# Kernel optimization log

Measured on AMD Instinct MI355X. Metric: run time of the kernel, lower is better.

## Reference

```python
import jax, jax.numpy as jnp
import numpy as np


def _sliding_window_attention(q, k, v, window_size, padding_mask):
    # q,k,v: [B,H,S,D]; faithful to the torch code incl. clamped scatter_add
    # duplicates at boundaries and the (score==0 -> -inf) quirk.
    B, H, S, D = q.shape
    hw = window_size // 2
    kp = jnp.pad(k, ((0, 0), (0, 0), (hw, hw), (0, 0)))  # zero-pad seq dim
    # window gather positions into padded keys: [S, W+1]
    pos = jnp.arange(S)[:, None] + jnp.arange(window_size + 1)[None, :]
    kw = kp[:, :, pos, :]  # [B,H,S,W+1,D]
    scores = jnp.einsum('bhsd,bhswd->bhsw', q, kw) / jnp.sqrt(jnp.asarray(D, q.dtype))
    # scatter-add into full [B,H,S,S] with clamped column indices (duplicates sum)
    idx = jnp.clip(jnp.arange(S)[:, None] + jnp.arange(-hw, hw + 1)[None, :], 0, S - 1)  # [S,W+1]
    rows = jnp.arange(S)[:, None]
    full = jnp.zeros((B, H, S, S), q.dtype).at[:, :, rows, idx].add(scores)
    neg_inf = jnp.asarray(-jnp.inf, full.dtype)
    full = jnp.where(full == 0.0, neg_inf, full)
    if padding_mask is not None:
        pm = padding_mask[:, None, None, :]  # [B,1,1,S]
        full = jnp.where(pm == 0, neg_inf, full)
        full = jnp.where(jnp.swapaxes(pm, -1, -2) == 0, neg_inf, full)
    att = jax.nn.softmax(full, axis=-1)
    att = jnp.where(jnp.isnan(att), jnp.asarray(0.0, att.dtype), att)
    values = jnp.einsum('bhst,bhtd->bhsd', att, v)
    return values, att


def setup_inputs() -> dict:
    key = jax.random.key(0)
    ks = jax.random.split(key, 5)
    B, S, IN_DIM, E = 2, 2048, 512, 512
    x = jax.random.normal(ks[0], (B, S, IN_DIM), dtype=jnp.float32)
    padding_mask = jnp.ones((B, S), dtype=jnp.int32)
    qkv_w = jax.random.normal(ks[1], (3 * E, IN_DIM), dtype=jnp.float32) * 0.02
    qkv_b = jnp.zeros((3 * E,), dtype=jnp.float32)
    o_w = jax.random.normal(ks[2], (E, E), dtype=jnp.float32) * 0.02
    o_b = jnp.zeros((E,), dtype=jnp.float32)
    return {'x': x, 'padding_mask': padding_mask, 'qkv_w': qkv_w, 'qkv_b': qkv_b,
            'o_w': o_w, 'o_b': o_b, 'window_size': 256, 'num_heads': 8}


def reference(x, padding_mask, qkv_w, qkv_b, o_w, o_b, window_size, num_heads):
    B, S, _ = x.shape
    E3 = qkv_w.shape[0]
    E = E3 // 3
    head_dim = E // num_heads
    qkv = x @ qkv_w.T + qkv_b                         # [B,S,3E]
    qkv = qkv.reshape(B, S, num_heads, 3 * head_dim)
    qkv = jnp.transpose(qkv, (0, 2, 1, 3))            # [B,H,S,3*hd]
    q, k, v = jnp.split(qkv, 3, axis=-1)
    values, _ = _sliding_window_attention(q, k, v, window_size, padding_mask)
    values = jnp.transpose(values, (0, 2, 1, 3)).reshape(B, S, E)
    o = values @ o_w.T + o_b
    return o
```

## Files before the change

### kernel.cpp

```cpp
#include <hip/hip_runtime.h>
#include <hip/hip_bf16.h>
#include <math.h>


typedef __bf16 bf16x8 __attribute__((ext_vector_type(8)));
typedef float f32x4 __attribute__((ext_vector_type(4)));

__device__ __forceinline__ unsigned short f2bf(float f) {
  unsigned u = __float_as_uint(f);
  unsigned r = u + 0x7FFFu + ((u >> 16) & 1u);
  return (unsigned short)(r >> 16);
}

__device__ __forceinline__ void ldsdma16(void* lds, const void* g) {
  __builtin_amdgcn_global_load_lds(
      (const __attribute__((address_space(1))) unsigned int*)g,
      (__attribute__((address_space(3))) unsigned int*)lds, 16, 0, 0);
}

__global__ __launch_bounds__(256) void cvt3_kernel(
    const float* __restrict__ s0, unsigned short* __restrict__ d0, int n0,
    const float* __restrict__ s1, unsigned short* __restrict__ d1, int n1,
    const float* __restrict__ s2, unsigned short* __restrict__ d2, int n2) {
  int i4 = blockIdx.x * 256 + threadIdx.x;
  const int c0 = n0 >> 2, c1 = (n0 + n1) >> 2, c2 = (n0 + n1 + n2) >> 2;
  const float* s; unsigned short* d; int base4;
  if (i4 < c0)      { s = s0; d = d0; base4 = i4; }
  else if (i4 < c1) { s = s1; d = d1; base4 = i4 - c0; }
  else if (i4 < c2) { s = s2; d = d2; base4 = i4 - c1; }
  else return;
  float4 v = ((const float4*)s)[base4];
  ushort4 o;
  o.x = f2bf(v.x); o.y = f2bf(v.y); o.z = f2bf(v.z); o.w = f2bf(v.w);
  ((ushort4*)d)[base4] = o;
}

__global__ __launch_bounds__(256) void gemm_qkv(
    const __hip_bfloat16* __restrict__ A, const __hip_bfloat16* __restrict__ Bw,
    const float* __restrict__ bias,
    __hip_bfloat16* __restrict__ qp, __hip_bfloat16* __restrict__ kpb,
    unsigned short* __restrict__ vtb) {
  __shared__ __hip_bfloat16 As[128 * 64];
  __shared__ __hip_bfloat16 Bs[96 * 64];

  const int tid = threadIdx.x, wave = tid >> 6, lane = tid & 63;
  const int m0 = blockIdx.x * 128, n0 = blockIdx.y * 96;
  const int wm = (wave >> 1) * 64, wn = (wave & 1) * 48;
  const int cl = lane & 15, ko = (lane >> 4) * 8;
  const int srow8 = lane >> 3;
  const int scol = 8 * ((lane & 7) ^ srow8);

  f32x4 acc[4][3] = {};

  for (int k0 = 0; k0 < 512; k0 += 64) {
    __syncthreads();
#pragma unroll
    for (int c = 0; c < 4; c++) {
      const int R = wave * 8 + c * 32;
      ldsdma16(&As[R * 64], A + (size_t)(m0 + R + srow8) * 512 + k0 + scol);
    }
#pragma unroll
    for (int c = 0; c < 3; c++) {
      const int R = wave * 8 + c * 32;
      ldsdma16(&Bs[R * 64], Bw + (size_t)(n0 + R + srow8) * 512 + k0 + scol);
    }
    __syncthreads();

#pragma unroll
    for (int ks = 0; ks < 2; ks++) {
      bf16x8 af[4], bf[3];
#pragma unroll
      for (int i = 0; i < 4; i++) {
        const int row = wm + cl + i * 16;
        af[i] = *(const bf16x8*)(&As[row * 64 + ((ks * 32 + ko) ^ ((row & 7) << 3))]);
      }
#pragma unroll
      for (int i = 0; i < 3; i++) {
        const int row = wn + cl + i * 16;
        bf[i] = *(const bf16x8*)(&Bs[row * 64 + ((ks * 32 + ko) ^ ((row & 7) << 3))]);
      }
#pragma unroll
      for (int mi = 0; mi < 4; mi++)
#pragma unroll
        for (int ni = 0; ni < 3; ni++)
          acc[mi][ni] = __builtin_amdgcn_mfma_f32_16x16x32_bf16(
              af[mi], bf[ni], acc[mi][ni], 0, 0, 0);
    }
  }

  const int crow = (lane >> 4) * 4;
#pragma unroll
  for (int mi = 0; mi < 4; mi++) {
    const int mb = m0 + wm + mi * 16 + crow;
    const int bq = mb >> 11, sl = mb & 2047;
#pragma unroll
    for (int ni = 0; ni < 3; ni++) {
      const int n = n0 + wn + ni * 16 + cl;
      const int h = n / 192;
      const int rem = n - h * 192;
      const int cat = rem >> 6;
      const int d = rem & 63;
      const float bv = bias[n];
      const size_t bh = (size_t)bq * 8 + h;
      if (cat == 2) {
        ushort4 o;
        o.x = f2bf(acc[mi][ni][0] + bv);
        o.y = f2bf(acc[mi][ni][1] + bv);
        o.z = f2bf(acc[mi][ni][2] + bv);
        o.w = f2bf(acc[mi][ni][3] + bv);
        *(ushort4*)(vtb + bh * 131072 + (sl >> 3) * 512 + d * 8 + (sl & 7)) = o;
      } else {
        __hip_bfloat16* dst = (cat == 0) ? qp : kpb;
        const float sc = (cat == 0) ? 0.18033688011112042f : 1.0f;
#pragma unroll
        for (int r = 0; r < 4; r++)
          dst[(bh * 2048 + sl + r) * 64 + d] =
              __float2bfloat16((acc[mi][ni][r] + bv) * sc);
      }
    }
  }
}

__global__ __launch_bounds__(256) void attn_mfma(
    const __hip_bfloat16* __restrict__ qp, const __hip_bfloat16* __restrict__ kp,
    const __hip_bfloat16* __restrict__ vt, const int* __restrict__ pm,
    __hip_bfloat16* __restrict__ vals) {
  __shared__ __hip_bfloat16 sKP[320 * 72];
  __shared__ float sCM[320];

  const int tid = threadIdx.x, wave = tid >> 6, lane = tid & 63;
  const int bid = blockIdx.x;
  const int s0 = (bid & 31) * 64;
  const int bh = bid >> 5;
  const int b = bh >> 3, h = bh & 7;
  const int t0 = s0 - 128;
  const int cl = lane & 15;
  const int g4 = (lane >> 4) * 4;
  const int ko = (lane >> 4) * 8;

  const __hip_bfloat16* qrow =
      qp + ((size_t)bh * 2048 + s0 + wave * 16 + cl) * 64 + ko;
  bf16x8 aq0 = *(const bf16x8*)(qrow);
  bf16x8 aq1 = *(const bf16x8*)(qrow + 32);

  {
    const int e = (tid & 7) * 8;
#pragma unroll
    for (int i = 0; i < 10; i++) {
      int row = (tid >> 3) + i * 32;
      int t = t0 + row; t = min(max(t, 0), 2047);
      *(uint4*)(&sKP[row * 72 + e]) =
          *(const uint4*)(kp + ((size_t)bh * 2048 + t) * 64 + e);
    }
  }
  for (int c = tid; c < 320; c += 256) {
    int t = t0 + c;
    bool ok = (t >= 0 && t < 2048) && (pm[b * 2048 + t] != 0);
    sCM[c] = ok ? 0.0f : -3.0e38f;
  }
  __syncthreads();

  f32x4 acc[17];
#pragma unroll
  for (int i = 0; i < 17; i++) {
    const int krow = (wave + i) * 16 + cl;
    bf16x8 b0 = *(const bf16x8*)(&sKP[krow * 72 + ko]);
    bf16x8 b1 = *(const bf16x8*)(&sKP[krow * 72 + ko + 32]);
    f32x4 z = {};
    z = __builtin_amdgcn_mfma_f32_16x16x32_bf16(aq0, b0, z, 0, 0, 0);
    acc[i] = __builtin_amdgcn_mfma_f32_16x16x32_bf16(aq1, b1, z, 0, 0, 0);
  }

  float lsum[4] = {0.f, 0.f, 0.f, 0.f};
#pragma unroll
  for (int i = 0; i < 17; i++) {
    const float ca = sCM[(wave + i) * 16 + cl];
#pragma unroll
    for (int r = 0; r < 4; r++) {
      float sv = acc[i][r] + ca;
      if (i == 0) {
        if (cl < g4 + r) sv = -3.0e38f;
      } else if (i == 16) {
        if (cl > g4 + r) sv = -3.0e38f;
      }
      float p = exp2f(sv);
      acc[i][r] = p;
      lsum[r] += p;
    }
  }
#pragma unroll
  for (int r = 0; r < 4; r++)
#pragma unroll
    for (int off = 1; off < 16; off <<= 1)
      lsum[r] += __shfl_xor(lsum[r], off);

  __syncthreads();

  __hip_bfloat16* sp = sKP + wave * 5248;
#pragma unroll
  for (int i = 0; i < 17; i++) {
    const int c = (wave + i) * 16 + cl;
#pragma unroll
    for (int r = 0; r < 4; r++)
      sp[(g4 + r) * 328 + c] = __float2bfloat16(acc[i][r]);
  }
  {
    const int zt = (wave & 1) ? (wave - 1) : (wave + 17);
    const int zc = zt * 16 + cl;
#pragma unroll
    for (int r = 0; r < 4; r++)
      sp[(g4 + r) * 328 + zc] = __float2bfloat16(0.f);
  }

  f32x4 oacc[4] = {};
  const int k0 = wave >> 1;
  const __hip_bfloat16* vbase = vt + (size_t)bh * 131072;
#pragma unroll
  for (int ks = 0; ks < 9; ks++) {
    const int kk = (k0 + ks) * 32 + ko;
    bf16x8 pa = *(const bf16x8*)(&sp[cl * 328 + kk]);
    int tv = t0 + kk; tv = min(max(tv, 0), 2040);
    const __hip_bfloat16* vrow = vbase + (tv >> 3) * 512;
#pragma unroll
    for (int ni = 0; ni < 4; ni++) {
      const int d = ni * 16 + cl;
      bf16x8 vb = *(const bf16x8*)(vrow + d * 8);
      oacc[ni] = __builtin_amdgcn_mfma_f32_16x16x32_bf16(pa, vb, oacc[ni], 0, 0, 0);
    }
  }

#pragma unroll
  for (int r = 0; r < 4; r++) {
    float linv = 1.0f / fmaxf(lsum[r], 1e-20f);
    const int qr = wave * 16 + g4 + r;
    if (sCM[qr + 128] != 0.0f) linv = 0.0f;
    const size_t obase = ((size_t)(b * 2048 + s0 + qr)) * 512 + h * 64 + cl;
#pragma unroll
    for (int ni = 0; ni < 4; ni++)
      vals[obase + ni * 16] = __float2bfloat16(oacc[ni][r] * linv);
  }
}

__global__ __launch_bounds__(256) void gemm_out(
    const __hip_bfloat16* __restrict__ A, const __hip_bfloat16* __restrict__ Bw,
    const float* __restrict__ bias, float* __restrict__ C) {
  __shared__ __hip_bfloat16 As[64 * 64];
  __shared__ __hip_bfloat16 Bs[64 * 64];

  const int tid = threadIdx.x, wave = tid >> 6, lane = tid & 63;
  const int m0 = blockIdx.x * 64, n0 = blockIdx.y * 64;
  const int wm = (wave >> 1) * 32, wn = (wave & 1) * 32;
  const int cl = lane & 15, ko = (lane >> 4) * 8;
  const int srow8 = lane >> 3;
  const int scol = 8 * ((lane & 7) ^ srow8);

  f32x4 acc[2][2] = {};

  for (int k0 = 0; k0 < 512; k0 += 64) {
    __syncthreads();
#pragma unroll
    for (int c = 0; c < 2; c++) {
      const int R = wave * 8 + c * 32;
      ldsdma16(&As[R * 64], A + (size_t)(m0 + R + srow8) * 512 + k0 + scol);
    }
#pragma unroll
    for (int c = 0; c < 2; c++) {
      const int R = wave * 8 + c * 32;
      ldsdma16(&Bs[R * 64], Bw + (size_t)(n0 + R + srow8) * 512 + k0 + scol);
    }
    __syncthreads();

#pragma unroll
    for (int ks = 0; ks < 2; ks++) {
      bf16x8 af[2], bf[2];
#pragma unroll
      for (int i = 0; i < 2; i++) {
        const int row = wm + cl + i * 16;
        af[i] = *(const bf16x8*)(&As[row * 64 + ((ks * 32 + ko) ^ ((row & 7) << 3))]);
      }
#pragma unroll
      for (int i = 0; i < 2; i++) {
        const int row = wn + cl + i * 16;
        bf[i] = *(const bf16x8*)(&Bs[row * 64 + ((ks * 32 + ko) ^ ((row & 7) << 3))]);
      }
#pragma unroll
      for (int mi = 0; mi < 2; mi++)
#pragma unroll
        for (int ni = 0; ni < 2; ni++)
          acc[mi][ni] = __builtin_amdgcn_mfma_f32_16x16x32_bf16(
              af[mi], bf[ni], acc[mi][ni], 0, 0, 0);
    }
  }

  const int crow = (lane >> 4) * 4;
#pragma unroll
  for (int mi = 0; mi < 2; mi++) {
#pragma unroll
    for (int ni = 0; ni < 2; ni++) {
      const int n = n0 + wn + ni * 16 + cl;
      const float bv = bias[n];
      const int mb = m0 + wm + mi * 16 + crow;
#pragma unroll
      for (int r = 0; r < 4; r++)
        C[(size_t)(mb + r) * 512 + n] = acc[mi][ni][r] + bv;
    }
  }
}

extern "C" void kernel_launch(void* const* d_in, const int* in_sizes, int n_in,
                              void* d_out, int out_size, void* d_ws, size_t ws_size,
                              hipStream_t stream) {
  const float* x     = (const float*)d_in[0];
  const int*   pm    = (const int*)d_in[1];
  const float* qkv_w = (const float*)d_in[2];
  const float* qkv_b = (const float*)d_in[3];
  const float* o_w   = (const float*)d_in[4];
  const float* o_b   = (const float*)d_in[5];
  float* out = (float*)d_out;

  __hip_bfloat16* wsb   = (__hip_bfloat16*)d_ws;
  __hip_bfloat16* xb    = wsb;
  __hip_bfloat16* wqkvb = wsb + 2097152;
  __hip_bfloat16* wob   = wsb + 2883584;
  __hip_bfloat16* qp    = wsb + 3145728;
  __hip_bfloat16* kp    = wsb + 5242880;
  __hip_bfloat16* vt    = wsb + 7340032;
  __hip_bfloat16* vals  = wsb + 9437184;

  dim3 blk(256);
  cvt3_kernel<<<dim3(3072), blk, 0, stream>>>(
      x, (unsigned short*)xb, 2097152,
      qkv_w, (unsigned short*)wqkvb, 786432,
      o_w, (unsigned short*)wob, 262144);
  gemm_qkv<<<dim3(32, 16), blk, 0, stream>>>(
      xb, wqkvb, qkv_b, qp, kp, (unsigned short*)vt);
  attn_mfma<<<dim3(512), blk, 0, stream>>>(qp, kp, vt, pm, vals);
  gemm_out<<<dim3(64, 8), blk, 0, stream>>>(vals, wob, o_b, out);
}
```

Before: 109.4 us.

## Load K tile via LDS DMA with XOR swizzle and transpose score MFMA

Loads the K window into LDS with global_load_lds DMA and an XOR-swizzled, unpadded layout instead of register-staged padded stores. The score MFMA operands are swapped so each lane holds four keys for one query. This turns the row-sum reduction into two cross-group shuffles and lets probabilities be stored as packed 4-wide bf16 writes. The aim is to cut LDS store traffic, bank conflicts and shuffle count in the attention kernel, at the cost of an extra shuffle per output row to fetch the sum.

```diff
diff --git a/kernel.cpp b/kernel.cpp
--- a/kernel.cpp
+++ b/kernel.cpp
@@ -144,13 +144,14 @@
   bf16x8 aq1 = *(const bf16x8*)(qrow + 32);
 
   {
-    const int e = (tid & 7) * 8;
+    const int srow8 = lane >> 3;
+    const int scol = 8 * ((lane & 7) ^ srow8);
 #pragma unroll
     for (int i = 0; i < 10; i++) {
-      int row = (tid >> 3) + i * 32;
-      int t = t0 + row; t = min(max(t, 0), 2047);
-      *(uint4*)(&sKP[row * 72 + e]) =
-          *(const uint4*)(kp + ((size_t)bh * 2048 + t) * 64 + e);
+      const int rbase = i * 32 + wave * 8;
+      int t = t0 + rbase + srow8;
+      t = min(max(t, 0), 2047);
+      ldsdma16(&sKP[rbase * 64], kp + ((size_t)bh * 2048 + t) * 64 + scol);
     }
   }
   for (int c = tid; c < 320; c += 256) {
@@ -164,52 +165,49 @@
 #pragma unroll
   for (int i = 0; i < 17; i++) {
     const int krow = (wave + i) * 16 + cl;
-    bf16x8 b0 = *(const bf16x8*)(&sKP[krow * 72 + ko]);
-    bf16x8 b1 = *(const bf16x8*)(&sKP[krow * 72 + ko + 32]);
+    const int kb = krow * 64;
+    const int sw = (cl & 7) << 3;
+    bf16x8 k0f = *(const bf16x8*)(&sKP[kb + (ko ^ sw)]);
+    bf16x8 k1f = *(const bf16x8*)(&sKP[kb + ((ko + 32) ^ sw)]);
     f32x4 z = {};
-    z = __builtin_amdgcn_mfma_f32_16x16x32_bf16(aq0, b0, z, 0, 0, 0);
-    acc[i] = __builtin_amdgcn_mfma_f32_16x16x32_bf16(aq1, b1, z, 0, 0, 0);
-  }
-
-  float lsum[4] = {0.f, 0.f, 0.f, 0.f};
+    z = __builtin_amdgcn_mfma_f32_16x16x32_bf16(k0f, aq0, z, 0, 0, 0);
+    acc[i] = __builtin_amdgcn_mfma_f32_16x16x32_bf16(k1f, aq1, z, 0, 0, 0);
+  }
+
+  float lsum = 0.f;
 #pragma unroll
   for (int i = 0; i < 17; i++) {
-    const float ca = sCM[(wave + i) * 16 + cl];
+    const f32x4 cm = *(const f32x4*)(&sCM[(wave + i) * 16 + g4]);
 #pragma unroll
     for (int r = 0; r < 4; r++) {
-      float sv = acc[i][r] + ca;
+      float sv = acc[i][r] + cm[r];
       if (i == 0) {
-        if (cl < g4 + r) sv = -3.0e38f;
+        if (g4 + r < cl) sv = -3.0e38f;
       } else if (i == 16) {
-        if (cl > g4 + r) sv = -3.0e38f;
+        if (g4 + r > cl) sv = -3.0e38f;
       }
       float p = exp2f(sv);
       acc[i][r] = p;
-      lsum[r] += p;
-    }
-  }
-#pragma unroll
-  for (int r = 0; r < 4; r++)
-#pragma unroll
-    for (int off = 1; off < 16; off <<= 1)
-      lsum[r] += __shfl_xor(lsum[r], off);
+      lsum += p;
+    }
+  }
+  lsum += __shfl_xor(lsum, 16);
+  lsum += __shfl_xor(lsum, 32);
 
   __syncthreads();
 
   __hip_bfloat16* sp = sKP + wave * 5248;
 #pragma unroll
   for (int i = 0; i < 17; i++) {
-    const int c = (wave + i) * 16 + cl;
-#pragma unroll
-    for (int r = 0; r < 4; r++)
-      sp[(g4 + r) * 328 + c] = __float2bfloat16(acc[i][r]);
+    ushort4 pk;
+    pk.x = f2bf(acc[i][0]); pk.y = f2bf(acc[i][1]);
+    pk.z = f2bf(acc[i][2]); pk.w = f2bf(acc[i][3]);
+    *(ushort4*)(&sp[cl * 328 + (wave + i) * 16 + g4]) = pk;
   }
   {
     const int zt = (wave & 1) ? (wave - 1) : (wave + 17);
-    const int zc = zt * 16 + cl;
-#pragma unroll
-    for (int r = 0; r < 4; r++)
-      sp[(g4 + r) * 328 + zc] = __float2bfloat16(0.f);
+    ushort4 zz = {0, 0, 0, 0};
+    *(ushort4*)(&sp[cl * 328 + zt * 16 + g4]) = zz;
   }
 
   f32x4 oacc[4] = {};
@@ -231,7 +229,8 @@
 
 #pragma unroll
   for (int r = 0; r < 4; r++) {
-    float linv = 1.0f / fmaxf(lsum[r], 1e-20f);
+    const float ls = __shfl(lsum, g4 + r);
+    float linv = 1.0f / fmaxf(ls, 1e-20f);
     const int qr = wave * 16 + g4 + r;
     if (sCM[qr + 128] != 0.0f) linv = 0.0f;
     const size_t obase = ((size_t)(b * 2048 + s0 + qr)) * 512 + h * 64 + cl;
```

Result: no change. 108.3 us (-1.0%).
